# Kernel tuning notes

Measured on AMD Instinct MI355X. Metric: run time of the kernel, lower is better.

## Reference

```python
import jax, jax.numpy as jnp
import numpy as np

N, E, F_IN, F_OUT = 8192, 1024, 256, 256


def setup_inputs() -> dict:
    key = jax.random.key(0)
    k1, k2, k3, k4 = jax.random.split(key, 4)
    X = jax.random.normal(k1, (N, F_IN), dtype=jnp.float32)
    # binary incidence matrix: node i belongs to hyperedge j with p=0.05
    H = (jax.random.uniform(k2, (N, E)) < 0.05).astype(jnp.float32)
    W = jax.random.normal(k3, (F_OUT, F_IN), dtype=jnp.float32) * (1.0 / np.sqrt(F_IN))
    b = jax.random.normal(k4, (F_OUT,), dtype=jnp.float32) * 0.01
    return {"X": X, "H": H, "W": W, "b": b}


def reference(X, H, W, b):
    # Dv = diag(row sums of H), De = diag(col sums of H)
    dv = jnp.sum(H, axis=1)                      # [N] node degrees
    de = jnp.sum(H, axis=0)                      # [E] edge degrees
    dv_inv_sqrt = 1.0 / jnp.sqrt(dv)             # inv of sqrt(Dv) (diagonal)
    de_inv = 1.0 / de                            # inv of De (diagonal)
    # diagonal matrices realized as broadcast scalings (same math, no N x N).
    Xs = X * dv_inv_sqrt[:, None]
    M = H.T @ Xs                                 # H^T (...)          [E, F]
    M = M * de_inv[:, None]                      # De^-1 (...)        [E, F]
    X_new = (H @ M) * dv_inv_sqrt[:, None]       # Dv^-1/2 H (...)    [N, F]
    return X_new @ W.T + b                       # nn.Linear
```

## Files before the change

kernel.cpp:

```cpp
#include <hip/hip_runtime.h>
#include <hip/hip_bf16.h>
#include <stdint.h>

typedef __attribute__((ext_vector_type(8))) short bf16x8;
typedef __attribute__((ext_vector_type(4))) float f32x4;
typedef __attribute__((ext_vector_type(4))) unsigned int u32x4;
typedef __attribute__((ext_vector_type(2))) unsigned int u32x2;
typedef unsigned short u16;
typedef unsigned int u32;
typedef unsigned long long u64;

#define N_NODES 8192
#define N_EDGES 1024
#define F_DIM   256
#define NMAX 128
#define EMAX 512
#define NSEG 256

__device__ __forceinline__ u16 f2bf(float f) {
    union { float f; u32 u; } v; v.f = f;
    u32 u = v.u;
    u = (u + 0x7FFFu + ((u >> 16) & 1u)) >> 16;
    return (u16)u;
}
__device__ __forceinline__ float bflo(u32 p) {
    union { u32 u; float f; } v; v.u = p << 16; return v.f;
}
__device__ __forceinline__ float bfhi(u32 p) {
    union { u32 u; float f; } v; v.u = p & 0xffff0000u; return v.f;
}

__global__ __launch_bounds__(512) void prep(
    const float* __restrict__ H, const float* __restrict__ X,
    float* __restrict__ dv, u16* __restrict__ nlist,
    u16* __restrict__ Xs, u32* __restrict__ HbT) {
    __shared__ u16 hmask[32][64];
    const int tid = threadIdx.x;
    const int wv = tid >> 6;
    const int lane = tid & 63;
    const int blk = blockIdx.x;
    const int n0 = blk * 32 + wv * 4;

    f32x4 hv[4][4], xv[4];
#pragma unroll
    for (int r = 0; r < 4; ++r) {
        const int n = n0 + r;
#pragma unroll
        for (int q = 0; q < 4; ++q)
            hv[r][q] = *(const f32x4*)(&H[(size_t)n * N_EDGES + q * 256 + lane * 4]);
        xv[r] = *(const f32x4*)(&X[(size_t)n * F_DIM + lane * 4]);
    }

#pragma unroll
    for (int r = 0; r < 4; ++r) {
        const int n = n0 + r;
        u32 m16 = 0u;
#pragma unroll
        for (int q = 0; q < 4; ++q)
#pragma unroll
            for (int j = 0; j < 4; ++j)
                m16 |= ((hv[r][q][j] != 0.f) ? 1u : 0u) << (q * 4 + j);
        hmask[wv * 4 + r][lane] = (u16)m16;
        const u32 cl = (u32)__popc(m16);
        u32 x = cl;
#pragma unroll
        for (int d = 1; d < 64; d <<= 1) {
            const u32 t = __shfl_up(x, d, 64);
            if (lane >= d) x += t;
        }
        const u32 total = __shfl(x, 63, 64);
        u32 pos = x - cl;
        u16* nrow = &nlist[(size_t)n * NMAX];
        u32 m = m16;
        while (m) {
            const int bidx = __builtin_ctz(m);
            m &= m - 1;
            const int col = ((bidx >> 2) << 8) + lane * 4 + (bidx & 3);
            if (pos < NMAX) nrow[pos] = (u16)col;
            ++pos;
        }
        if (lane == 0) dv[n] = (float)total;
        const float s = rsqrtf((float)total);
        u32x2 pk;
        pk[0] = (u32)f2bf(xv[r][0] * s) | ((u32)f2bf(xv[r][1] * s) << 16);
        pk[1] = (u32)f2bf(xv[r][2] * s) | ((u32)f2bf(xv[r][3] * s) << 16);
        *(u32x2*)(&Xs[(size_t)n * F_DIM + lane * 4]) = pk;
    }
    __syncthreads();
#pragma unroll
    for (int eo = 0; eo < 2; ++eo) {
        const int e = tid + eo * 512;
        const int widx = (e & 255) >> 2;
        const int bit = ((e >> 8) << 2) + (e & 3);
        u32 w = 0u;
#pragma unroll
        for (int r = 0; r < 32; ++r)
            w |= (u32)((hmask[r][widx] >> bit) & 1u) << r;
        HbT[(size_t)e * NSEG + blk] = w;
    }
}

__global__ __launch_bounds__(512) void spmm1(
    const u16* __restrict__ Xs, const u32* __restrict__ HbT,
    u16* __restrict__ Mb) {
    __shared__ u32 words[NSEG];
    __shared__ u16 lst[EMAX];
    __shared__ u32 wtot[4];
    __shared__ float red[16][2][128];
    const int tid = threadIdx.x;
    const int wv = tid >> 6;
    const int lane = tid & 63;
    const int e = blockIdx.x;
    if (tid < NSEG) words[tid] = HbT[(size_t)e * NSEG + tid];
    __syncthreads();
    u32 c = 0, x = 0;
    if (tid < NSEG) {
        c = (u32)__popc(words[tid]);
        x = c;
#pragma unroll
        for (int d = 1; d < 64; d <<= 1) {
            const u32 t = __shfl_up(x, d, 64);
            if (lane >= d) x += t;
        }
        if (lane == 63) wtot[wv] = x;
    }
    __syncthreads();
    if (tid < NSEG) {
        u32 off = 0;
        for (int w = 0; w < wv; ++w) off += wtot[w];
        u32 pos = off + x - c;
        u32 m = words[tid];
        const int nb = tid * 32;
        while (m) {
            const int b = __builtin_ctz(m);
            m &= m - 1;
            if (pos < EMAX) lst[pos] = (u16)(nb + b);
            ++pos;
        }
    }
    __syncthreads();
    const u32 de = wtot[0] + wtot[1] + wtot[2] + wtot[3];
    const int cnt = min((int)de, EMAX);
    const int half = lane >> 5, l32 = lane & 31;
    const int npairs = (cnt + 1) >> 1;
    const int len = (npairs + 7) >> 3;
    const int p0 = wv * len;
    const int p1 = min(p0 + len, npairs);
    float a[8] = {};
#pragma unroll 8
    for (int p = p0; p < p1; ++p) {
        const int idx = 2 * p + half;
        if (idx < cnt) {
            const int n = lst[idx];
            const u32x4 pk = *(const u32x4*)(&Xs[(size_t)n * F_DIM + l32 * 8]);
            a[0] += bflo(pk[0]); a[1] += bfhi(pk[0]);
            a[2] += bflo(pk[1]); a[3] += bfhi(pk[1]);
            a[4] += bflo(pk[2]); a[5] += bfhi(pk[2]);
            a[6] += bflo(pk[3]); a[7] += bfhi(pk[3]);
        }
    }
    const int ws = wv * 2 + half;
    f32x4 r0 = {a[0], a[1], a[2], a[3]};
    f32x4 r1 = {a[4], a[5], a[6], a[7]};
    *(f32x4*)(&red[ws][0][l32 * 4]) = r0;
    *(f32x4*)(&red[ws][1][l32 * 4]) = r1;
    __syncthreads();
    if (tid < F_DIM) {
        const int f = tid;
        const int pl = (f >> 2) & 1;
        const int ix = ((f >> 3) << 2) | (f & 3);
        float s = 0.f;
#pragma unroll
        for (int w = 0; w < 16; ++w) s += red[w][pl][ix];
        Mb[(size_t)e * F_DIM + f] = f2bf(s / (float)de);
    }
}

__global__ __launch_bounds__(256) void spmm2w(
    const u16* __restrict__ Mb, const float* __restrict__ dv,
    const u16* __restrict__ nlist, const float* __restrict__ W,
    const float* __restrict__ bias, float* __restrict__ out) {
    __shared__ u16 nl[16 * NMAX];
    __shared__ u16 Yb[16][264];
    __shared__ float redA[4][2][256];
    const int tid = threadIdx.x;
    const int wv = tid >> 6;
    const int lane = tid & 63;
    const int n0 = blockIdx.x * 16;
    {
        const u32* gn = (const u32*)&nlist[(size_t)n0 * NMAX];
#pragma unroll
        for (int k = 0; k < 4; ++k)
            ((u32*)nl)[tid + k * 256] = gn[tid + k * 256];
    }
    __syncthreads();
    const int half = lane >> 5, l32 = lane & 31;
#pragma unroll
    for (int r = 0; r < 4; ++r) {
        const int row = wv * 4 + r;
        const int n = n0 + row;
        const float dvn = dv[n];
        const int cnt = min((int)dvn, NMAX);
        const u16* lt = &nl[row * NMAX];
        float a[8] = {};
        const int npairs = (cnt + 1) >> 1;
#pragma unroll 8
        for (int p = 0; p < npairs; ++p) {
            const int idx = 2 * p + half;
            if (idx < cnt) {
                const int e = lt[idx];
                const u32x4 pk = *(const u32x4*)(&Mb[(size_t)e * F_DIM + l32 * 8]);
                a[0] += bflo(pk[0]); a[1] += bfhi(pk[0]);
                a[2] += bflo(pk[1]); a[3] += bfhi(pk[1]);
                a[4] += bflo(pk[2]); a[5] += bfhi(pk[2]);
                a[6] += bflo(pk[3]); a[7] += bfhi(pk[3]);
            }
        }
        f32x4 v0 = {a[0], a[1], a[2], a[3]};
        f32x4 v1 = {a[4], a[5], a[6], a[7]};
        *(f32x4*)(&redA[wv][half][l32 * 8]) = v0;
        *(f32x4*)(&redA[wv][half][l32 * 8 + 4]) = v1;
        const float s = rsqrtf(dvn);
        const f32x4 u0 = *(const f32x4*)(&redA[wv][0][lane * 4]);
        const f32x4 u1 = *(const f32x4*)(&redA[wv][1][lane * 4]);
        u32x2 pk;
        pk[0] = (u32)f2bf((u0[0] + u1[0]) * s) | ((u32)f2bf((u0[1] + u1[1]) * s) << 16);
        pk[1] = (u32)f2bf((u0[2] + u1[2]) * s) | ((u32)f2bf((u0[3] + u1[3]) * s) << 16);
        *(u32x2*)(&Yb[row][lane * 4]) = pk;
    }
    __syncthreads();
    const int row16 = lane & 15, quad = lane >> 4;
    const int jbase = wv * 64;
    f32x4 acc[4] = {};
    for (int ko = 0; ko < 256; ko += 32) {
        const bf16x8 af = *(const bf16x8*)(&Yb[row16][ko + quad * 8]);
#pragma unroll
        for (int tn = 0; tn < 4; ++tn) {
            const int j = jbase + tn * 16 + row16;
            const f32x4 w0 = *(const f32x4*)(&W[(size_t)j * F_DIM + ko + quad * 8]);
            const f32x4 w1 = *(const f32x4*)(&W[(size_t)j * F_DIM + ko + quad * 8 + 4]);
            union { u32x4 u; bf16x8 b; } bf;
            bf.u[0] = (u32)f2bf(w0[0]) | ((u32)f2bf(w0[1]) << 16);
            bf.u[1] = (u32)f2bf(w0[2]) | ((u32)f2bf(w0[3]) << 16);
            bf.u[2] = (u32)f2bf(w1[0]) | ((u32)f2bf(w1[1]) << 16);
            bf.u[3] = (u32)f2bf(w1[2]) | ((u32)f2bf(w1[3]) << 16);
            acc[tn] = __builtin_amdgcn_mfma_f32_16x16x32_bf16(af, bf.b, acc[tn], 0, 0, 0);
        }
    }
#pragma unroll
    for (int tn = 0; tn < 4; ++tn) {
        const int col = jbase + tn * 16 + row16;
        const float bc = bias[col];
#pragma unroll
        for (int r2 = 0; r2 < 4; ++r2) {
            const int n = n0 + quad * 4 + r2;
            out[(size_t)n * F_DIM + col] = acc[tn][r2] + bc;
        }
    }
}

extern "C" void kernel_launch(void* const* d_in, const int* in_sizes, int n_in,
                              void* d_out, int out_size, void* d_ws, size_t ws_size,
                              hipStream_t stream) {
    (void)in_sizes; (void)n_in; (void)out_size; (void)ws_size;
    const float* X = (const float*)d_in[0];
    const float* H = (const float*)d_in[1];
    const float* W = (const float*)d_in[2];
    const float* b = (const float*)d_in[3];
    float* out = (float*)d_out;

    char* ws = (char*)d_ws;
    float* dv    = (float*)(ws);
    u32*   HbT   = (u32*)(ws + 0x10000);
    u16*   nlist = (u16*)(ws + 0x110000);
    u16*   Xs    = (u16*)(ws + 0x310000);
    u16*   Mb    = (u16*)(ws + 0x710000);

    prep<<<NSEG, 512, 0, stream>>>(H, X, dv, nlist, Xs, HbT);
    spmm1<<<N_EDGES, 512, 0, stream>>>(Xs, HbT, Mb);
    spmm2w<<<N_NODES / 16, 256, 0, stream>>>(Mb, dv, nlist, W, b, out);
}
```

Measured before the change: 145.7 us.

## Pre-convert W to bf16 in prep and restructure spmm2w to one row per wave

The prep kernel now also converts W to bf16 once (one row per block via wave 7), so the final kernel loads bf16 weights directly instead of converting fp32 W in every block. spmm2w now handles 8 nodes per 512-thread block with one node per wave, reducing halves with a shuffle instead of shared-memory round trips, and runs the MFMA with half the A rows zero-padded. Both gather loops replace the per-iteration branch with clamped index and a multiplicative mask to avoid divergence. The MFMA tile is half-wasted and W is re-read by more blocks.

```diff
diff --git a/kernel.cpp b/kernel.cpp
--- a/kernel.cpp
+++ b/kernel.cpp
@@ -32,8 +32,9 @@
 
 __global__ __launch_bounds__(512) void prep(
     const float* __restrict__ H, const float* __restrict__ X,
+    const float* __restrict__ W,
     float* __restrict__ dv, u16* __restrict__ nlist,
-    u16* __restrict__ Xs, u32* __restrict__ HbT) {
+    u16* __restrict__ Xs, u32* __restrict__ HbT, u16* __restrict__ Wb) {
     __shared__ u16 hmask[32][64];
     const int tid = threadIdx.x;
     const int wv = tid >> 6;
@@ -49,6 +50,14 @@
         for (int q = 0; q < 4; ++q)
             hv[r][q] = *(const f32x4*)(&H[(size_t)n * N_EDGES + q * 256 + lane * 4]);
         xv[r] = *(const f32x4*)(&X[(size_t)n * F_DIM + lane * 4]);
+    }
+
+    if (wv == 7) {
+        const f32x4 w = *(const f32x4*)(&W[(size_t)blk * F_DIM + lane * 4]);
+        u32x2 pk;
+        pk[0] = (u32)f2bf(w[0]) | ((u32)f2bf(w[1]) << 16);
+        pk[1] = (u32)f2bf(w[2]) | ((u32)f2bf(w[3]) << 16);
+        *(u32x2*)(&Wb[(size_t)blk * F_DIM + lane * 4]) = pk;
     }
 
 #pragma unroll
@@ -149,15 +158,15 @@
     float a[8] = {};
 #pragma unroll 8
     for (int p = p0; p < p1; ++p) {
-        const int idx = 2 * p + half;
-        if (idx < cnt) {
-            const int n = lst[idx];
-            const u32x4 pk = *(const u32x4*)(&Xs[(size_t)n * F_DIM + l32 * 8]);
-            a[0] += bflo(pk[0]); a[1] += bfhi(pk[0]);
-            a[2] += bflo(pk[1]); a[3] += bfhi(pk[1]);
-            a[4] += bflo(pk[2]); a[5] += bfhi(pk[2]);
-            a[6] += bflo(pk[3]); a[7] += bfhi(pk[3]);
-        }
+        const int idx0 = 2 * p + half;
+        const int idx = min(idx0, cnt - 1);
+        const float msk = (idx0 < cnt) ? 1.f : 0.f;
+        const int n = lst[idx];
+        const u32x4 pk = *(const u32x4*)(&Xs[(size_t)n * F_DIM + l32 * 8]);
+        a[0] = fmaf(bflo(pk[0]), msk, a[0]); a[1] = fmaf(bfhi(pk[0]), msk, a[1]);
+        a[2] = fmaf(bflo(pk[1]), msk, a[2]); a[3] = fmaf(bfhi(pk[1]), msk, a[3]);
+        a[4] = fmaf(bflo(pk[2]), msk, a[4]); a[5] = fmaf(bfhi(pk[2]), msk, a[5]);
+        a[6] = fmaf(bflo(pk[3]), msk, a[6]); a[7] = fmaf(bfhi(pk[3]), msk, a[7]);
     }
     const int ws = wv * 2 + half;
     f32x4 r0 = {a[0], a[1], a[2], a[3]};
@@ -176,85 +185,71 @@
     }
 }
 
-__global__ __launch_bounds__(256) void spmm2w(
+__global__ __launch_bounds__(512) void spmm2w(
     const u16* __restrict__ Mb, const float* __restrict__ dv,
-    const u16* __restrict__ nlist, const float* __restrict__ W,
+    const u16* __restrict__ nlist, const u16* __restrict__ Wb,
     const float* __restrict__ bias, float* __restrict__ out) {
-    __shared__ u16 nl[16 * NMAX];
-    __shared__ u16 Yb[16][264];
-    __shared__ float redA[4][2][256];
+    __shared__ u16 nl[8 * NMAX];
+    __shared__ u16 Yb[8][264];
     const int tid = threadIdx.x;
     const int wv = tid >> 6;
     const int lane = tid & 63;
-    const int n0 = blockIdx.x * 16;
-    {
-        const u32* gn = (const u32*)&nlist[(size_t)n0 * NMAX];
-#pragma unroll
-        for (int k = 0; k < 4; ++k)
-            ((u32*)nl)[tid + k * 256] = gn[tid + k * 256];
-    }
+    const int n0 = blockIdx.x * 8;
+    ((u32*)nl)[tid] = ((const u32*)&nlist[(size_t)n0 * NMAX])[tid];
     __syncthreads();
     const int half = lane >> 5, l32 = lane & 31;
-#pragma unroll
-    for (int r = 0; r < 4; ++r) {
-        const int row = wv * 4 + r;
-        const int n = n0 + row;
-        const float dvn = dv[n];
-        const int cnt = min((int)dvn, NMAX);
-        const u16* lt = &nl[row * NMAX];
-        float a[8] = {};
-        const int npairs = (cnt + 1) >> 1;
+    const int n = n0 + wv;
+    const float dvn = dv[n];
+    const int cnt = min((int)dvn, NMAX);
+    const u16* lt = &nl[wv * NMAX];
+    float a[8] = {};
+    const int npairs = (cnt + 1) >> 1;
 #pragma unroll 8
-        for (int p = 0; p < npairs; ++p) {
-            const int idx = 2 * p + half;
-            if (idx < cnt) {
-                const int e = lt[idx];
-                const u32x4 pk = *(const u32x4*)(&Mb[(size_t)e * F_DIM + l32 * 8]);
-                a[0] += bflo(pk[0]); a[1] += bfhi(pk[0]);
-                a[2] += bflo(pk[1]); a[3] += bfhi(pk[1]);
-                a[4] += bflo(pk[2]); a[5] += bfhi(pk[2]);
-                a[6] += bflo(pk[3]); a[7] += bfhi(pk[3]);
-            }
-        }
-        f32x4 v0 = {a[0], a[1], a[2], a[3]};
-        f32x4 v1 = {a[4], a[5], a[6], a[7]};
-        *(f32x4*)(&redA[wv][half][l32 * 8]) = v0;
-        *(f32x4*)(&redA[wv][half][l32 * 8 + 4]) = v1;
-        const float s = rsqrtf(dvn);
-        const f32x4 u0 = *(const f32x4*)(&redA[wv][0][lane * 4]);
-        const f32x4 u1 = *(const f32x4*)(&redA[wv][1][lane * 4]);
-        u32x2 pk;
-        pk[0] = (u32)f2bf((u0[0] + u1[0]) * s) | ((u32)f2bf((u0[1] + u1[1]) * s) << 16);
-        pk[1] = (u32)f2bf((u0[2] + u1[2]) * s) | ((u32)f2bf((u0[3] + u1[3]) * s) << 16);
-        *(u32x2*)(&Yb[row][lane * 4]) = pk;
+    for (int p = 0; p < npairs; ++p) {
+        const int idx0 = 2 * p + half;
+        const int idx = min(idx0, cnt - 1);
+        const float msk = (idx0 < cnt) ? 1.f : 0.f;
+        const int e = lt[idx];
+        const u32x4 pk = *(const u32x4*)(&Mb[(size_t)e * F_DIM + l32 * 8]);
+        a[0] = fmaf(bflo(pk[0]), msk, a[0]); a[1] = fmaf(bfhi(pk[0]), msk, a[1]);
+        a[2] = fmaf(bflo(pk[1]), msk, a[2]); a[3] = fmaf(bfhi(pk[1]), msk, a[3]);
+        a[4] = fmaf(bflo(pk[2]), msk, a[4]); a[5] = fmaf(bfhi(pk[2]), msk, a[5]);
+        a[6] = fmaf(bflo(pk[3]), msk, a[6]); a[7] = fmaf(bfhi(pk[3]), msk, a[7]);
+    }
+#pragma unroll
+    for (int k = 0; k < 8; ++k) a[k] += __shfl_xor(a[k], 32, 64);
+    const float s = rsqrtf(dvn);
+    if (half == 0) {
+        u32x4 pk;
+        pk[0] = (u32)f2bf(a[0] * s) | ((u32)f2bf(a[1] * s) << 16);
+        pk[1] = (u32)f2bf(a[2] * s) | ((u32)f2bf(a[3] * s) << 16);
+        pk[2] = (u32)f2bf(a[4] * s) | ((u32)f2bf(a[5] * s) << 16);
+        pk[3] = (u32)f2bf(a[6] * s) | ((u32)f2bf(a[7] * s) << 16);
+        *(u32x4*)(&Yb[wv][l32 * 8]) = pk;
     }
     __syncthreads();
     const int row16 = lane & 15, quad = lane >> 4;
-    const int jbase = wv * 64;
-    f32x4 acc[4] = {};
+    f32x4 acc[2] = {};
     for (int ko = 0; ko < 256; ko += 32) {
-        const bf16x8 af = *(const bf16x8*)(&Yb[row16][ko + quad * 8]);
-#pragma unroll
-        for (int tn = 0; tn < 4; ++tn) {
-            const int j = jbase + tn * 16 + row16;
-            const f32x4 w0 = *(const f32x4*)(&W[(size_t)j * F_DIM + ko + quad * 8]);
-            const f32x4 w1 = *(const f32x4*)(&W[(size_t)j * F_DIM + ko + quad * 8 + 4]);
-            union { u32x4 u; bf16x8 b; } bf;
-            bf.u[0] = (u32)f2bf(w0[0]) | ((u32)f2bf(w0[1]) << 16);
-            bf.u[1] = (u32)f2bf(w0[2]) | ((u32)f2bf(w0[3]) << 16);
-            bf.u[2] = (u32)f2bf(w1[0]) | ((u32)f2bf(w1[1]) << 16);
-            bf.u[3] = (u32)f2bf(w1[2]) | ((u32)f2bf(w1[3]) << 16);
-            acc[tn] = __builtin_amdgcn_mfma_f32_16x16x32_bf16(af, bf.b, acc[tn], 0, 0, 0);
-        }
-    }
-#pragma unroll
-    for (int tn = 0; tn < 4; ++tn) {
-        const int col = jbase + tn * 16 + row16;
+        bf16x8 af = {};
+        if (row16 < 8)
+            af = *(const bf16x8*)(&Yb[row16][ko + quad * 8]);
+#pragma unroll
+        for (int tn = 0; tn < 2; ++tn) {
+            const int j = wv * 32 + tn * 16 + row16;
+            const bf16x8 bf = *(const bf16x8*)(&Wb[(size_t)j * F_DIM + ko + quad * 8]);
+            acc[tn] = __builtin_amdgcn_mfma_f32_16x16x32_bf16(af, bf, acc[tn], 0, 0, 0);
+        }
+    }
+#pragma unroll
+    for (int tn = 0; tn < 2; ++tn) {
+        const int col = wv * 32 + tn * 16 + row16;
         const float bc = bias[col];
 #pragma unroll
         for (int r2 = 0; r2 < 4; ++r2) {
-            const int n = n0 + quad * 4 + r2;
-            out[(size_t)n * F_DIM + col] = acc[tn][r2] + bc;
+            const int row = quad * 4 + r2;
+            if (row < 8)
+                out[(size_t)(n0 + row) * F_DIM + col] = acc[tn][r2] + bc;
         }
     }
 }
@@ -275,8 +270,9 @@
     u16*   nlist = (u16*)(ws + 0x110000);
     u16*   Xs    = (u16*)(ws + 0x310000);
     u16*   Mb    = (u16*)(ws + 0x710000);
-
-    prep<<<NSEG, 512, 0, stream>>>(H, X, dv, nlist, Xs, HbT);
+    u16*   Wb    = (u16*)(ws + 0x790000);
+
+    prep<<<NSEG, 512, 0, stream>>>(H, X, W, dv, nlist, Xs, HbT, Wb);
     spmm1<<<N_EDGES, 512, 0, stream>>>(Xs, HbT, Mb);
-    spmm2w<<<N_NODES / 16, 256, 0, stream>>>(Mb, dv, nlist, W, b, out);
-}
+    spmm2w<<<N_NODES / 8, 512, 0, stream>>>(Mb, dv, nlist, Wb, b, out);
+}
```

Measured after the change: 134.4 us. 7.8% less time.
